# Kernel optimization log

Hardware: AMD Instinct MI355X
Metric: run time of the kernel (lower is better)

The kernel has to match this reference:

```python
import jax, jax.numpy as jnp
import numpy as np

B, F, K = 8192, 4096, 64


def setup_inputs() -> dict:
    key = jax.random.key(0)
    kx, kv = jax.random.split(key)
    x = jax.random.normal(kx, (B, F), dtype=jnp.float32)
    # original init: uniform(-0.01, 0.01)
    v = jax.random.uniform(kv, (F, K), dtype=jnp.float32, minval=-0.01, maxval=0.01)
    return {"x": x, "v": v}


def reference(x, v):
    # sum_{i<j} <v_i, v_j> x_i x_j  ==  0.5 * sum_f ((x@v)_f^2 - (x^2 @ v^2)_f)
    xv = x @ v                      # [B, K]
    x2v2 = (x * x) @ (v * v)        # [B, K]
    res = 0.5 * jnp.sum(xv * xv - x2v2, axis=-1, keepdims=True)  # [B, 1]
    return res
```

## Files before the change

kernel.cpp:

```cpp
#include <hip/hip_runtime.h>
#include <hip/hip_bf16.h>


#define F_DIM 4096
#define K_DIM 64
#define B_ROWS 8192

typedef __attribute__((ext_vector_type(8))) short short8;
typedef __attribute__((ext_vector_type(4))) float float4v;
typedef __attribute__((ext_vector_type(16))) float f32x16;

__device__ __forceinline__ short f2bs(float f) {
    __hip_bfloat16 h = __float2bfloat16(f);
    short s;
    __builtin_memcpy(&s, &h, 2);
    return s;
}

__global__ void prep_kernel(const float* __restrict__ v,
                            __hip_bfloat16* __restrict__ vt,
                            float* __restrict__ w) {
    const int wave = (blockIdx.x * blockDim.x + threadIdx.x) >> 6;
    const int lane = threadIdx.x & 63;
    if (wave >= F_DIM) return;
    const float val = v[wave * K_DIM + lane];
    float sq = val * val;
#pragma unroll
    for (int m = 32; m >= 1; m >>= 1) sq += __shfl_xor(sq, m, 64);
    if (lane == 0) w[wave] = sq;
    vt[(size_t)lane * F_DIM + wave] = __float2bfloat16(val);
}

__launch_bounds__(1024, 4)
__global__ void fm_main_kernel(const float* __restrict__ x,
                               const __hip_bfloat16* __restrict__ vt,
                               const float* __restrict__ w,
                               float* __restrict__ out) {
    __shared__ float yred[8][32][64];
    __shared__ float s1s[32];
    __shared__ float s2s[32];

    const int tid  = threadIdx.x;
    const int lane = tid & 63;
    const int wid  = tid >> 6;
    const int lrow = lane & 31;
    const int lk8  = (lane >> 5) * 8;
    const int row0 = blockIdx.x * 32;

    if (tid < 32) s2s[tid] = 0.0f;
    __syncthreads();

    const float* xrow = x + (size_t)(row0 + lrow) * F_DIM;
    const int fbase = wid * (F_DIM / 16);

    f32x16 acc0{};
    f32x16 acc1{};
    float s2p = 0.0f;

#pragma unroll 2
    for (int ks = 0; ks < 16; ++ks) {
        const int fo = fbase + ks * 16 + lk8;
        const float4v xa = *(const float4v*)(xrow + fo);
        const float4v xb = *(const float4v*)(xrow + fo + 4);
        const float4v wa = *(const float4v*)(w + fo);
        const float4v wb = *(const float4v*)(w + fo + 4);

        s2p += xa.x*xa.x*wa.x + xa.y*xa.y*wa.y + xa.z*xa.z*wa.z + xa.w*xa.w*wa.w
             + xb.x*xb.x*wb.x + xb.y*xb.y*wb.y + xb.z*xb.z*wb.z + xb.w*xb.w*wb.w;

        short8 af;
        af[0]=f2bs(xa.x); af[1]=f2bs(xa.y); af[2]=f2bs(xa.z); af[3]=f2bs(xa.w);
        af[4]=f2bs(xb.x); af[5]=f2bs(xb.y); af[6]=f2bs(xb.z); af[7]=f2bs(xb.w);

        const __hip_bfloat16* bb = vt + fo;
        const short8 b0 = *(const short8*)(bb + (size_t)lrow * F_DIM);
        const short8 b1 = *(const short8*)(bb + (size_t)(32 + lrow) * F_DIM);

        acc0 = __builtin_amdgcn_mfma_f32_32x32x16_bf16(af, b0, acc0, 0, 0, 0);
        acc1 = __builtin_amdgcn_mfma_f32_32x32x16_bf16(af, b1, acc1, 0, 0, 0);
    }

    s2p += __shfl_xor(s2p, 32, 64);
    if (lane < 32) atomicAdd(&s2s[lrow], s2p);

    const int rbase = 4 * (lane >> 5);
    if (wid < 8) {
#pragma unroll
        for (int r = 0; r < 16; ++r) {
            const int row = (r & 3) + 8 * (r >> 2) + rbase;
            yred[wid][row][lrow]      = acc0[r];
            yred[wid][row][32 + lrow] = acc1[r];
        }
    }
    __syncthreads();
    if (wid >= 8) {
#pragma unroll
        for (int r = 0; r < 16; ++r) {
            const int row = (r & 3) + 8 * (r >> 2) + rbase;
            yred[wid - 8][row][lrow]      += acc0[r];
            yred[wid - 8][row][32 + lrow] += acc1[r];
        }
    }
    __syncthreads();

#pragma unroll
    for (int h = 0; h < 2; ++h) {
        const int row = 2 * wid + h;
        float y = 0.0f;
#pragma unroll
        for (int s = 0; s < 8; ++s) y += yred[s][row][lane];
        float yy = y * y;
#pragma unroll
        for (int m = 32; m >= 1; m >>= 1) yy += __shfl_xor(yy, m, 64);
        if (lane == 0) s1s[row] = yy;
    }
    __syncthreads();

    if (tid < 32) out[row0 + tid] = 0.5f * (s1s[tid] - s2s[tid]);
}

extern "C" void kernel_launch(void* const* d_in, const int* in_sizes, int n_in,
                              void* d_out, int out_size, void* d_ws, size_t ws_size,
                              hipStream_t stream) {
    const float* x = (const float*)d_in[0];
    const float* v = (const float*)d_in[1];
    float* out = (float*)d_out;

    __hip_bfloat16* vt = (__hip_bfloat16*)d_ws;
    float* w = (float*)((char*)d_ws + (size_t)K_DIM * F_DIM * 2);

    prep_kernel<<<F_DIM / 4, 256, 0, stream>>>(v, vt, w);
    fm_main_kernel<<<B_ROWS / 32, 1024, 0, stream>>>(x, vt, w, out);
}
```

Before: 213.1 us.

## Pre-swizzle V into MFMA fragment order so B loads are contiguous

```diff
diff --git a/kernel.cpp b/kernel.cpp
--- a/kernel.cpp
+++ b/kernel.cpp
@@ -18,22 +18,45 @@
 }
 
 __global__ void prep_kernel(const float* __restrict__ v,
-                            __hip_bfloat16* __restrict__ vt,
+                            short* __restrict__ vtf,
                             float* __restrict__ w) {
-    const int wave = (blockIdx.x * blockDim.x + threadIdx.x) >> 6;
+    __shared__ short lds_t[4][64][16];
+
+    const int wid  = threadIdx.x >> 6;
     const int lane = threadIdx.x & 63;
-    if (wave >= F_DIM) return;
-    const float val = v[wave * K_DIM + lane];
-    float sq = val * val;
+    const int fc   = blockIdx.x * 4 + wid;
+    const int r    = lane >> 2;
+    const int k0   = (lane & 3) * 16;
+
+    const float* src = v + (size_t)(fc * 16 + r) * K_DIM + k0;
+    float vals[16];
 #pragma unroll
-    for (int m = 32; m >= 1; m >>= 1) sq += __shfl_xor(sq, m, 64);
-    if (lane == 0) w[wave] = sq;
-    vt[(size_t)lane * F_DIM + wave] = __float2bfloat16(val);
+    for (int i = 0; i < 16; i += 4) {
+        float4v t = *(const float4v*)(src + i);
+        vals[i] = t.x; vals[i+1] = t.y; vals[i+2] = t.z; vals[i+3] = t.w;
+    }
+
+    float sq = 0.0f;
+#pragma unroll
+    for (int i = 0; i < 16; ++i) sq += vals[i] * vals[i];
+    sq += __shfl_xor(sq, 1, 64);
+    sq += __shfl_xor(sq, 2, 64);
+    if ((lane & 3) == 0) w[fc * 16 + r] = sq;
+
+#pragma unroll
+    for (int kk = 0; kk < 16; ++kk) lds_t[wid][k0 + kk][r] = f2bs(vals[kk]);
+    __syncthreads();
+
+#pragma unroll
+    for (int c = 0; c < 2; ++c) {
+        const short8 frag = *(const short8*)&lds_t[wid][c * 32 + (lane & 31)][8 * (lane >> 5)];
+        *(short8*)(vtf + ((size_t)fc * 2 + c) * 512 + lane * 8) = frag;
+    }
 }
 
 __launch_bounds__(1024, 4)
 __global__ void fm_main_kernel(const float* __restrict__ x,
-                               const __hip_bfloat16* __restrict__ vt,
+                               const short* __restrict__ vtf,
                                const float* __restrict__ w,
                                float* __restrict__ out) {
     __shared__ float yred[8][32][64];
@@ -52,6 +75,7 @@
 
     const float* xrow = x + (size_t)(row0 + lrow) * F_DIM;
     const int fbase = wid * (F_DIM / 16);
+    const int fcbase = fbase >> 4;
 
     f32x16 acc0{};
     f32x16 acc1{};
@@ -72,9 +96,9 @@
         af[0]=f2bs(xa.x); af[1]=f2bs(xa.y); af[2]=f2bs(xa.z); af[3]=f2bs(xa.w);
         af[4]=f2bs(xb.x); af[5]=f2bs(xb.y); af[6]=f2bs(xb.z); af[7]=f2bs(xb.w);
 
-        const __hip_bfloat16* bb = vt + fo;
-        const short8 b0 = *(const short8*)(bb + (size_t)lrow * F_DIM);
-        const short8 b1 = *(const short8*)(bb + (size_t)(32 + lrow) * F_DIM);
+        const size_t fc = (size_t)(fcbase + ks) * 2;
+        const short8 b0 = *(const short8*)(vtf + (fc + 0) * 512 + lane * 8);
+        const short8 b1 = *(const short8*)(vtf + (fc + 1) * 512 + lane * 8);
 
         acc0 = __builtin_amdgcn_mfma_f32_32x32x16_bf16(af, b0, acc0, 0, 0, 0);
         acc1 = __builtin_amdgcn_mfma_f32_32x32x16_bf16(af, b1, acc1, 0, 0, 0);
@@ -126,9 +150,9 @@
     const float* v = (const float*)d_in[1];
     float* out = (float*)d_out;
 
-    __hip_bfloat16* vt = (__hip_bfloat16*)d_ws;
+    short* vtf = (short*)d_ws;
     float* w = (float*)((char*)d_ws + (size_t)K_DIM * F_DIM * 2);
 
-    prep_kernel<<<F_DIM / 4, 256, 0, stream>>>(v, vt, w);
-    fm_main_kernel<<<B_ROWS / 32, 1024, 0, stream>>>(x, vt, w, out);
+    prep_kernel<<<F_DIM / 16 / 4, 256, 0, stream>>>(v, vtf, w);
+    fm_main_kernel<<<B_ROWS / 32, 1024, 0, stream>>>(x, vtf, w, out);
 }
```

Result: faster. 203.3 us (-4.6%).
